# Optimization experiments

Measured on AMD Instinct MI355X. Metric: run time of the kernel, lower is better.

The kernel has to match this reference:

```python
import jax, jax.numpy as jnp
import numpy as np

WINDOW = 4
EPS = 1e-5


def setup_inputs() -> dict:
    key = jax.random.key(0)
    ks = jax.random.split(key, 12)
    B, T, D = 2, 4096, 1024
    H = D // 2
    s = 0.02
    return {
        "x": jax.random.normal(ks[0], (B, T, D), dtype=jnp.float32),
        # tension_net: Linear(2D -> D/2), SiLU, Linear(D/2 -> 1). Weights stored [in, out].
        "w1": jax.random.normal(ks[1], (2 * D, H), dtype=jnp.float32) * s,
        "b1": jnp.zeros((H,), dtype=jnp.float32),
        "w2": jax.random.normal(ks[2], (H, 1), dtype=jnp.float32) * s,
        "b2": jnp.zeros((1,), dtype=jnp.float32),
        # wv: Linear(D -> D)
        "wv_w": jax.random.normal(ks[3], (D, D), dtype=jnp.float32) * s,
        "wv_b": jnp.zeros((D,), dtype=jnp.float32),
        # merge: Linear(2D -> D)
        "merge_w": jax.random.normal(ks[4], (2 * D, D), dtype=jnp.float32) * s,
        "merge_b": jnp.zeros((D,), dtype=jnp.float32),
        # LayerNorm(D)
        "gamma": jnp.ones((D,), dtype=jnp.float32),
        "beta": jnp.zeros((D,), dtype=jnp.float32),
    }


def reference(x, w1, b1, w2, b2, wv_w, wv_b, merge_w, merge_b, gamma, beta):
    B, T, D = x.shape
    W = WINDOW
    # Causal sliding-window neighbor gather: nb[:, t, w] = x[:, t-w-1] if t-w-1 >= 0 else 0.
    idx = jnp.arange(T)[:, None] - jnp.arange(W)[None, :] - 1          # [T, W]
    valid = (idx >= 0)                                                  # [T, W]
    nb = jnp.take(x, jnp.clip(idx, 0, None), axis=1)                   # [B, T, W, D]
    nb = jnp.where(valid[None, :, :, None], nb, jnp.zeros((), x.dtype))
    # Pairwise tension gate: tiny MLP on [h_t, nb].
    h_t = jnp.broadcast_to(x[:, :, None, :], (B, T, W, D))
    pair = jnp.concatenate([h_t, nb], axis=-1)                          # [B, T, W, 2D]
    hid = jax.nn.silu(jnp.einsum('btwe,eh->btwh', pair, w1) + b1)       # [B, T, W, D/2]
    tau = jax.nn.sigmoid((jnp.einsum('btwh,ho->btwo', hid, w2) + b2)[..., 0])  # [B, T, W]
    # Value projection of neighbors (note: zero-padded neighbors still get wv bias, matching torch).
    v = jnp.einsum('btwd,de->btwe', nb, wv_w) + wv_b                    # [B, T, W, D]
    msg = jnp.einsum('btw,btwd->btd', tau, v)                           # [B, T, D]
    # Merge + LayerNorm.
    y = jnp.einsum('bte,ed->btd', jnp.concatenate([x, msg], axis=-1), merge_w) + merge_b
    mu = jnp.mean(y, axis=-1, keepdims=True)
    var = jnp.mean(jnp.square(y - mu), axis=-1, keepdims=True)
    y = (y - mu) * jax.lax.rsqrt(var + EPS) * gamma + beta
    return y
```

## Files before the change

kernel.cpp:

```cpp
#include <hip/hip_runtime.h>
#include <hip/hip_bf16.h>

#define TT 4096
#define TD 1024
#define TM 8192
#define CN 3072
#define EPS 1e-5f

typedef __bf16 bf16;
typedef __bf16 bf16x4 __attribute__((ext_vector_type(4)));
typedef __bf16 bf16x8 __attribute__((ext_vector_type(8)));
typedef float  f32x4  __attribute__((ext_vector_type(4)));

#define GLOBAL_AS __attribute__((address_space(1)))
#define LDS_AS    __attribute__((address_space(3)))

__global__ __launch_bounds__(256) void prep_kernel(const float* __restrict__ x,
                                                   const float* __restrict__ w1,
                                                   const float* __restrict__ wv_w,
                                                   const float* __restrict__ wv_b,
                                                   const float* __restrict__ merge_w,
                                                   bf16* __restrict__ Xbf,
                                                   bf16* __restrict__ BigBT,
                                                   bf16* __restrict__ Amb,
                                                   bf16* __restrict__ WvBf,
                                                   float* __restrict__ cvecP) {
    __shared__ float tile[32][33];
    int b = blockIdx.x;
    const int tid = threadIdx.x;

    if (b < 16) {
        const int j = (b & 3) * 256 + tid;
        const int e0 = (b >> 2) * 256;
        const float* col = merge_w + (size_t)(1024 + e0) * 1024 + j;
        float acc = 0.f;
#pragma unroll 32
        for (int e = 0; e < 256; ++e) acc += wv_b[e0 + e] * col[(size_t)e * 1024];
        cvecP[(b >> 2) * 1024 + j] = acc;
        return;
    }
    b -= 16;
    if (b < 8192) {
        int i = b * 256 + tid;
        float4 v = ((const float4*)x)[i];
        bf16x4 o; o[0] = (bf16)v.x; o[1] = (bf16)v.y; o[2] = (bf16)v.z; o[3] = (bf16)v.w;
        *(bf16x4*)(Xbf + (size_t)i * 4) = o;
        return;
    }
    b -= 8192;

    const float* src; bf16* dst; int srcN, tilesX, dstOff;
    if (b < 512)       {            src = w1;                        srcN = 512;  tilesX = 16; dst = BigBT; dstOff = 0;    }
    else if (b < 1024) { b -= 512;  src = w1 + (size_t)1024 * 512;   srcN = 512;  tilesX = 16; dst = BigBT; dstOff = 512;  }
    else if (b < 2048) { b -= 1024; src = merge_w;                   srcN = 1024; tilesX = 32; dst = BigBT; dstOff = 2048; }
    else if (b < 3072) { b -= 2048; src = merge_w + (size_t)1024 * 1024; srcN = 1024; tilesX = 32; dst = Amb; dstOff = 0; }
    else {
        b -= 3072;
        int i = b * 256 + tid;
        float4 v = ((const float4*)wv_w)[i];
        bf16x4 o; o[0] = (bf16)v.x; o[1] = (bf16)v.y; o[2] = (bf16)v.z; o[3] = (bf16)v.w;
        *(bf16x4*)(WvBf + (size_t)i * 4) = o;
        return;
    }
    int n0 = (b % tilesX) * 32, k0 = (b / tilesX) * 32;
    int tx = tid & 31, ty = tid >> 5;
#pragma unroll
    for (int r = 0; r < 32; r += 8)
        tile[ty + r][tx] = src[(size_t)(k0 + ty + r) * srcN + n0 + tx];
    __syncthreads();
#pragma unroll
    for (int r = 0; r < 32; r += 8)
        dst[(size_t)(dstOff + n0 + ty + r) * 1024 + k0 + tx] = (bf16)tile[tx][ty + r];
}

__global__ __launch_bounds__(256) void wprime_kernel(const bf16* __restrict__ Amb,
                                                     const bf16* __restrict__ WvBf,
                                                     bf16* __restrict__ Wout,
                                                     const float* __restrict__ cvecP,
                                                     float* __restrict__ cvec) {
    int b = blockIdx.x;
    if (b == 256) {
        int j = threadIdx.x * 4;
        float4 s0 = *(const float4*)(cvecP + j);
        float4 s1 = *(const float4*)(cvecP + 1024 + j);
        float4 s2 = *(const float4*)(cvecP + 2048 + j);
        float4 s3 = *(const float4*)(cvecP + 3072 + j);
        float4 o = {s0.x + s1.x + s2.x + s3.x, s0.y + s1.y + s2.y + s3.y,
                    s0.z + s1.z + s2.z + s3.z, s0.w + s1.w + s2.w + s3.w};
        *(float4*)(cvec + j) = o;
        return;
    }
    __shared__ bf16 As[64 * 64];
    __shared__ bf16 Bs[64 * 64];
    const int m0 = (b >> 4) * 64;
    const int n0 = (b & 15) * 64;
    const int tid = threadIdx.x;
    const int wave = tid >> 6, lane = tid & 63;
    const int wr = (wave >> 1) * 32, wc = (wave & 1) * 32;
    const int lrow = lane & 15, cbase = lane >> 4;
    const int sw = lrow & 7;

    f32x4 acc[2][2] = {};

    for (int k0 = 0; k0 < 1024; k0 += 64) {
        __syncthreads();
#pragma unroll
        for (int c = 0; c < 2; ++c) {
            int e = (c * 256 + tid) * 8;
            int row = e >> 6;
            int q = (e >> 3) & 7;
            int gcol = ((q ^ (row & 7)) << 3);
            const bf16* ga = Amb  + (size_t)(m0 + row) * 1024 + k0 + gcol;
            const bf16* gb = WvBf + (size_t)(n0 + row) * 1024 + k0 + gcol;
            __builtin_amdgcn_global_load_lds((const GLOBAL_AS void*)ga,
                                             (LDS_AS void*)(As + e), 16, 0, 0);
            __builtin_amdgcn_global_load_lds((const GLOBAL_AS void*)gb,
                                             (LDS_AS void*)(Bs + e), 16, 0, 0);
        }
        __syncthreads();

#pragma unroll
        for (int kk = 0; kk < 2; ++kk) {
            const int qo = ((cbase + kk * 4) ^ sw) << 3;
            bf16x8 af[2], bfr[2];
#pragma unroll
            for (int i = 0; i < 2; ++i) {
                af[i]  = *(const bf16x8*)(As + (wr + i * 16 + lrow) * 64 + qo);
                bfr[i] = *(const bf16x8*)(Bs + (wc + i * 16 + lrow) * 64 + qo);
            }
#pragma unroll
            for (int i = 0; i < 2; ++i)
#pragma unroll
                for (int j = 0; j < 2; ++j)
                    acc[i][j] = __builtin_amdgcn_mfma_f32_16x16x32_bf16(af[i], bfr[j], acc[i][j], 0, 0, 0);
        }
    }

    const int lr = (lane >> 4) * 4, lc = lane & 15;
#pragma unroll
    for (int i = 0; i < 2; ++i)
#pragma unroll
        for (int j = 0; j < 2; ++j)
#pragma unroll
            for (int r = 0; r < 4; ++r)
                Wout[(size_t)(m0 + wr + i * 16 + lr + r) * 1024 + (n0 + wc + j * 16 + lc)]
                    = (bf16)acc[i][j][r];
}

#define MFMA16(a, b, c) __builtin_amdgcn_mfma_f32_16x16x32_bf16((a), (b), (c), 0, 0, 0)

#define STAGE_A(BUF, T, L0, L1) do {                                              \
    _Pragma("unroll")                                                             \
    for (int ld_ = (L0); ld_ < (L1); ++ld_) {                                     \
        const bf16* ga_ = aBase + (size_t)(ld_ * 32) * 1024 + (T) * 64;           \
        __builtin_amdgcn_global_load_lds((const GLOBAL_AS void*)ga_,              \
            (LDS_AS void*)(SMEM + (BUF) * 28672 + ld_ * 2048 + tid * 8), 16, 0, 0); \
    } } while (0)

#define STAGE_B(BUF, T, L0, L1) do {                                              \
    _Pragma("unroll")                                                             \
    for (int ld_ = (L0); ld_ < (L1); ++ld_) {                                     \
        const bf16* gb_ = bBase + (size_t)(ld_ * 32) * 1024 + (T) * 64;           \
        __builtin_amdgcn_global_load_lds((const GLOBAL_AS void*)gb_,              \
            (LDS_AS void*)(SMEM + (BUF) * 28672 + 16384 + ld_ * 2048 + tid * 8), 16, 0, 0); \
    } } while (0)

#define AF(BUF, I, KK) (*(const bf16x8*)(SMEM + (BUF) * 28672 +                   \
    (wm * 128 + (I) * 16 + lrow) * 64 + (((cbase + (KK) * 4) ^ sw) << 3)))
#define BF(BUF, J, KK) (*(const bf16x8*)(SMEM + (BUF) * 28672 + 16384 +           \
    (wn * 96 + (J) * 16 + lrow) * 64 + (((cbase + (KK) * 4) ^ sw) << 3)))

#define NOSTAGE do {} while (0)
#define NOGATE  do {} while (0)
#define GATE0 do { asm volatile("s_waitcnt vmcnt(0)" ::: "memory");               \
                   __builtin_amdgcn_sched_barrier(0); } while (0)

#define PH(BUF, KK, H, RDB, STAGE, GATE) do {                                     \
    if (RDB) {                                                                    \
        _Pragma("unroll")                                                         \
        for (int j = 0; j < 6; ++j) bfr[j] = BF(BUF, j, KK);                      \
    }                                                                             \
    bf16x8 a0_ = AF(BUF, (H) * 4 + 0, KK);                                        \
    bf16x8 a1_ = AF(BUF, (H) * 4 + 1, KK);                                        \
    bf16x8 a2_ = AF(BUF, (H) * 4 + 2, KK);                                        \
    bf16x8 a3_ = AF(BUF, (H) * 4 + 3, KK);                                        \
    STAGE;                                                                        \
    __builtin_amdgcn_s_barrier();                                                 \
    __builtin_amdgcn_sched_barrier(0);                                            \
    __builtin_amdgcn_s_setprio(1);                                                \
    _Pragma("unroll")                                                             \
    for (int j = 0; j < 6; ++j) {                                                 \
        acc[(H) * 4 + 0][j] = MFMA16(a0_, bfr[j], acc[(H) * 4 + 0][j]);           \
        acc[(H) * 4 + 1][j] = MFMA16(a1_, bfr[j], acc[(H) * 4 + 1][j]);           \
        acc[(H) * 4 + 2][j] = MFMA16(a2_, bfr[j], acc[(H) * 4 + 2][j]);           \
        acc[(H) * 4 + 3][j] = MFMA16(a3_, bfr[j], acc[(H) * 4 + 3][j]);           \
    }                                                                             \
    __builtin_amdgcn_s_setprio(0);                                                \
    GATE;                                                                         \
    __builtin_amdgcn_s_barrier();                                                 \
    __builtin_amdgcn_sched_barrier(0);                                            \
} while (0)

#define TILE(BUF, S0, S1, S2, G3)                                                 \
    PH(BUF, 0, 0, 1, S0, NOGATE);                                                 \
    PH(BUF, 0, 1, 0, S1, NOGATE);                                                 \
    PH(BUF, 1, 0, 1, S2, NOGATE);                                                 \
    PH(BUF, 1, 1, 0, NOSTAGE, G3);

__global__ __launch_bounds__(256, 1) void gemm_big(const bf16* __restrict__ A,
                                                   const bf16* __restrict__ BT,
                                                   bf16* __restrict__ C) {
    __shared__ __align__(16) bf16 SMEM[57344];
    const int NB = 3072, K = 1024;

    const int L = blockIdx.x;
    const int m0 = (L >> 4) * 256;
    const int n0 = ((L & 7) * 2 + ((L >> 3) & 1)) * 192;
    const int tid = threadIdx.x;
    const int wave = tid >> 6, lane = tid & 63;
    const int wm = wave >> 1;
    const int wn = wave & 1;
    const int lrow = lane & 15, cbase = lane >> 4;
    const int sw = lrow & 7;

    const int r0 = tid >> 3;
    const int c0 = ((tid & 7) ^ ((tid >> 3) & 7)) << 3;
    const bf16* aBase = A  + (size_t)(m0 + r0) * K + c0;
    const bf16* bBase = BT + (size_t)(n0 + r0) * K + c0;

    f32x4 acc[8][6] = {};
    bf16x8 bfr[6];

    STAGE_A(0, 0, 0, 8);
    STAGE_B(0, 0, 0, 6);
    asm volatile("s_waitcnt vmcnt(0)" ::: "memory");
    __builtin_amdgcn_sched_barrier(0);
    __builtin_amdgcn_s_barrier();
    __builtin_amdgcn_sched_barrier(0);

    for (int i = 0; i < 7; ++i) {
        const int t1 = 2 * i + 1, t2 = 2 * i + 2;
        TILE(0, STAGE_A(1, t1, 0, 4), STAGE_A(1, t1, 4, 8), STAGE_B(1, t1, 0, 6), GATE0);
        TILE(1, STAGE_A(0, t2, 0, 4), STAGE_A(0, t2, 4, 8), STAGE_B(0, t2, 0, 6), GATE0);
    }
    TILE(0, STAGE_A(1, 15, 0, 4), STAGE_A(1, 15, 4, 8), STAGE_B(1, 15, 0, 6), GATE0);
    TILE(1, NOSTAGE, NOSTAGE, NOSTAGE, NOGATE);

    __syncthreads();
    bf16* ep = SMEM + wave * 6656;
    const int lr = (lane >> 4) * 4, lc = lane & 15;
#pragma unroll
    for (int h = 0; h < 2; ++h) {
#pragma unroll
        for (int ii = 0; ii < 4; ++ii)
#pragma unroll
            for (int j = 0; j < 6; ++j)
#pragma unroll
                for (int r = 0; r < 4; ++r)
                    ep[(ii * 16 + lr + r) * 104 + (j * 16 + lc)]
                        = (bf16)acc[h * 4 + ii][j][r];
        __syncthreads();
        bf16* Cw = C + (size_t)(m0 + wm * 128 + h * 64) * NB + n0 + wn * 96;
#pragma unroll
        for (int p = 0; p < 8; ++p) {
            int R = p * 8 + (lane >> 3);
            int Ccol = (lane & 7) * 8;
            bf16x8 v = *(const bf16x8*)(ep + R * 104 + Ccol);
            *(bf16x8*)(Cw + (size_t)R * NB + Ccol) = v;
        }
#pragma unroll
        for (int p = 0; p < 4; ++p) {
            int R = p * 16 + (lane >> 2);
            int Ccol = 64 + (lane & 3) * 8;
            bf16x8 v = *(const bf16x8*)(ep + R * 104 + Ccol);
            *(bf16x8*)(Cw + (size_t)R * NB + Ccol) = v;
        }
        __syncthreads();
    }
}

__global__ __launch_bounds__(256) void final_kernel(const bf16* __restrict__ C,
                                                    const float* __restrict__ b1,
                                                    const float* __restrict__ b2,
                                                    const float* __restrict__ w2,
                                                    const float* __restrict__ cvec,
                                                    const float* __restrict__ merge_b,
                                                    const float* __restrict__ gamma,
                                                    const float* __restrict__ beta,
                                                    float* __restrict__ out) {
    const int wave = threadIdx.x >> 6, lane = threadIdx.x & 63;
    const int row = blockIdx.x * 4 + wave;
    const int t = row & (TT - 1);
    const bf16* Crow = C + (size_t)row * CN;

    const int h0 = lane * 8;
    bf16x8 u8 = *(const bf16x8*)(Crow + h0);
    float4 b1a = *(const float4*)(b1 + h0), b1b = *(const float4*)(b1 + h0 + 4);
    float4 w2a = *(const float4*)(w2 + h0), w2b = *(const float4*)(w2 + h0 + 4);
    float u[8] = {(float)u8[0] + b1a.x, (float)u8[1] + b1a.y,
                  (float)u8[2] + b1a.z, (float)u8[3] + b1a.w,
                  (float)u8[4] + b1b.x, (float)u8[5] + b1b.y,
                  (float)u8[6] + b1b.z, (float)u8[7] + b1b.w};
    const float w2v[8] = {w2a.x, w2a.y, w2a.z, w2a.w, w2b.x, w2b.y, w2b.z, w2b.w};

    float partial[4];
#pragma unroll
    for (int w = 0; w < 4; ++w) {
        float p = 0.f;
        if (t >= w + 1) {
            bf16x8 v8 = *(const bf16x8*)(C + (size_t)(row - w - 1) * CN + 512 + h0);
#pragma unroll
            for (int k = 0; k < 8; ++k) {
                float z = u[k] + (float)v8[k];
                p += (z / (1.f + __expf(-z))) * w2v[k];
            }
        } else {
#pragma unroll
            for (int k = 0; k < 8; ++k) {
                float z = u[k];
                p += (z / (1.f + __expf(-z))) * w2v[k];
            }
        }
        partial[w] = p;
    }
#pragma unroll
    for (int w = 0; w < 4; ++w)
#pragma unroll
        for (int off = 1; off < 64; off <<= 1)
            partial[w] += __shfl_xor(partial[w], off, 64);

    const float bias2 = b2[0];
    float taus[4];
#pragma unroll
    for (int w = 0; w < 4; ++w)
        taus[w] = 1.f / (1.f + __expf(-(partial[w] + bias2)));
    const float tsum = taus[0] + taus[1] + taus[2] + taus[3];

    const int d0 = lane * 16;
    bf16x8 y1a = *(const bf16x8*)(Crow + 2048 + d0);
    bf16x8 y1b = *(const bf16x8*)(Crow + 2048 + d0 + 8);
    float v[16];
#pragma unroll
    for (int k = 0; k < 8; ++k) { v[k] = (float)y1a[k]; v[8 + k] = (float)y1b[k]; }
#pragma unroll
    for (int q = 0; q < 4; ++q) {
        float4 cv = *(const float4*)(cvec + d0 + q * 4);
        float4 mb = *(const float4*)(merge_b + d0 + q * 4);
        v[q*4+0] += tsum * cv.x + mb.x; v[q*4+1] += tsum * cv.y + mb.y;
        v[q*4+2] += tsum * cv.z + mb.z; v[q*4+3] += tsum * cv.w + mb.w;
    }
#pragma unroll
    for (int w = 0; w < 4; ++w) {
        if (t >= w + 1) {
            const bf16* Pn = C + (size_t)(row - w - 1) * CN + 1024 + d0;
            bf16x8 pa = *(const bf16x8*)Pn;
            bf16x8 pb = *(const bf16x8*)(Pn + 8);
#pragma unroll
            for (int k = 0; k < 8; ++k) {
                v[k] += taus[w] * (float)pa[k];
                v[8 + k] += taus[w] * (float)pb[k];
            }
        }
    }

    float s = 0.f, ss = 0.f;
#pragma unroll
    for (int k = 0; k < 16; ++k) { s += v[k]; ss += v[k] * v[k]; }
#pragma unroll
    for (int off = 1; off < 64; off <<= 1) {
        s  += __shfl_xor(s, off, 64);
        ss += __shfl_xor(ss, off, 64);
    }
    const float mu = s * (1.f / TD);
    const float var = ss * (1.f / TD) - mu * mu;
    const float r = rsqrtf(var + EPS);

#pragma unroll
    for (int q = 0; q < 4; ++q) {
        float4 g  = *(const float4*)(gamma + d0 + q * 4);
        float4 bt = *(const float4*)(beta + d0 + q * 4);
        float4 o;
        o.x = (v[q*4+0] - mu) * r * g.x + bt.x;
        o.y = (v[q*4+1] - mu) * r * g.y + bt.y;
        o.z = (v[q*4+2] - mu) * r * g.z + bt.z;
        o.w = (v[q*4+3] - mu) * r * g.w + bt.w;
        *(float4*)(out + (size_t)row * TD + d0 + q * 4) = o;
    }
}

extern "C" void kernel_launch(void* const* d_in, const int* in_sizes, int n_in,
                              void* d_out, int out_size, void* d_ws, size_t ws_size,
                              hipStream_t stream) {
    const float* x       = (const float*)d_in[0];
    const float* w1      = (const float*)d_in[1];
    const float* b1      = (const float*)d_in[2];
    const float* w2      = (const float*)d_in[3];
    const float* b2      = (const float*)d_in[4];
    const float* wv_w    = (const float*)d_in[5];
    const float* wv_b    = (const float*)d_in[6];
    const float* merge_w = (const float*)d_in[7];
    const float* merge_b = (const float*)d_in[8];
    const float* gamma   = (const float*)d_in[9];
    const float* beta    = (const float*)d_in[10];
    float* out = (float*)d_out;

    char* ws = (char*)d_ws;
    bf16*  Xbf   = (bf16*)ws;  ws += (size_t)TM * 1024 * 2;
    bf16*  BigBT = (bf16*)ws;  ws += (size_t)CN * 1024 * 2;
    bf16*  Amb   = (bf16*)ws;  ws += (size_t)1024 * 1024 * 2;
    bf16*  WvBf  = (bf16*)ws;  ws += (size_t)1024 * 1024 * 2;
    float* cvecP = (float*)ws; ws += (size_t)4 * 1024 * 4;
    float* cvec  = (float*)ws; ws += (size_t)1024 * 4;
    bf16*  Cbuf  = (bf16*)ws;

    prep_kernel<<<12304, 256, 0, stream>>>(x, w1, wv_w, wv_b, merge_w,
                                           Xbf, BigBT, Amb, WvBf, cvecP);

    wprime_kernel<<<257, 256, 0, stream>>>(Amb, WvBf, BigBT + (size_t)1024 * 1024,
                                           cvecP, cvec);

    gemm_big<<<512, 256, 0, stream>>>(Xbf, BigBT, Cbuf);

    final_kernel<<<TM / 4, 256, 0, stream>>>(Cbuf, b1, b2, w2, cvec, merge_b,
                                             gamma, beta, out);
}
```

Measured before the change: 202.9 us.

## Use 512-thread blocks with 8 waves splitting the GEMM tile

```diff
diff --git a/kernel.cpp b/kernel.cpp
--- a/kernel.cpp
+++ b/kernel.cpp
@@ -149,24 +149,24 @@
 
 #define MFMA16(a, b, c) __builtin_amdgcn_mfma_f32_16x16x32_bf16((a), (b), (c), 0, 0, 0)
 
-#define STAGE_A(BUF, T, L0, L1) do {                                              \
+#define STAGE_A(BUF, T) do {                                                      \
     _Pragma("unroll")                                                             \
-    for (int ld_ = (L0); ld_ < (L1); ++ld_) {                                     \
-        const bf16* ga_ = aBase + (size_t)(ld_ * 32) * 1024 + (T) * 64;           \
+    for (int ld_ = 0; ld_ < 4; ++ld_) {                                           \
+        const bf16* ga_ = aBase + (size_t)(ld_ * 64) * 1024 + (T) * 64;           \
         __builtin_amdgcn_global_load_lds((const GLOBAL_AS void*)ga_,              \
-            (LDS_AS void*)(SMEM + (BUF) * 28672 + ld_ * 2048 + tid * 8), 16, 0, 0); \
+            (LDS_AS void*)(SMEM + (BUF) * 28672 + ld_ * 4096 + tid * 8), 16, 0, 0); \
     } } while (0)
 
-#define STAGE_B(BUF, T, L0, L1) do {                                              \
+#define STAGE_B(BUF, T) do {                                                      \
     _Pragma("unroll")                                                             \
-    for (int ld_ = (L0); ld_ < (L1); ++ld_) {                                     \
-        const bf16* gb_ = bBase + (size_t)(ld_ * 32) * 1024 + (T) * 64;           \
+    for (int ld_ = 0; ld_ < 3; ++ld_) {                                           \
+        const bf16* gb_ = bBase + (size_t)(ld_ * 64) * 1024 + (T) * 64;           \
         __builtin_amdgcn_global_load_lds((const GLOBAL_AS void*)gb_,              \
-            (LDS_AS void*)(SMEM + (BUF) * 28672 + 16384 + ld_ * 2048 + tid * 8), 16, 0, 0); \
+            (LDS_AS void*)(SMEM + (BUF) * 28672 + 16384 + ld_ * 4096 + tid * 8), 16, 0, 0); \
     } } while (0)
 
 #define AF(BUF, I, KK) (*(const bf16x8*)(SMEM + (BUF) * 28672 +                   \
-    (wm * 128 + (I) * 16 + lrow) * 64 + (((cbase + (KK) * 4) ^ sw) << 3)))
+    (wm * 64 + (I) * 16 + lrow) * 64 + (((cbase + (KK) * 4) ^ sw) << 3)))
 #define BF(BUF, J, KK) (*(const bf16x8*)(SMEM + (BUF) * 28672 + 16384 +           \
     (wn * 96 + (J) * 16 + lrow) * 64 + (((cbase + (KK) * 4) ^ sw) << 3)))
 
@@ -180,20 +180,16 @@
         _Pragma("unroll")                                                         \
         for (int j = 0; j < 6; ++j) bfr[j] = BF(BUF, j, KK);                      \
     }                                                                             \
-    bf16x8 a0_ = AF(BUF, (H) * 4 + 0, KK);                                        \
-    bf16x8 a1_ = AF(BUF, (H) * 4 + 1, KK);                                        \
-    bf16x8 a2_ = AF(BUF, (H) * 4 + 2, KK);                                        \
-    bf16x8 a3_ = AF(BUF, (H) * 4 + 3, KK);                                        \
+    bf16x8 a0_ = AF(BUF, (H) * 2 + 0, KK);                                        \
+    bf16x8 a1_ = AF(BUF, (H) * 2 + 1, KK);                                        \
     STAGE;                                                                        \
     __builtin_amdgcn_s_barrier();                                                 \
     __builtin_amdgcn_sched_barrier(0);                                            \
     __builtin_amdgcn_s_setprio(1);                                                \
     _Pragma("unroll")                                                             \
     for (int j = 0; j < 6; ++j) {                                                 \
-        acc[(H) * 4 + 0][j] = MFMA16(a0_, bfr[j], acc[(H) * 4 + 0][j]);           \
-        acc[(H) * 4 + 1][j] = MFMA16(a1_, bfr[j], acc[(H) * 4 + 1][j]);           \
-        acc[(H) * 4 + 2][j] = MFMA16(a2_, bfr[j], acc[(H) * 4 + 2][j]);           \
-        acc[(H) * 4 + 3][j] = MFMA16(a3_, bfr[j], acc[(H) * 4 + 3][j]);           \
+        acc[(H) * 2 + 0][j] = MFMA16(a0_, bfr[j], acc[(H) * 2 + 0][j]);           \
+        acc[(H) * 2 + 1][j] = MFMA16(a1_, bfr[j], acc[(H) * 2 + 1][j]);           \
     }                                                                             \
     __builtin_amdgcn_s_setprio(0);                                                \
     GATE;                                                                         \
@@ -201,13 +197,13 @@
     __builtin_amdgcn_sched_barrier(0);                                            \
 } while (0)
 
-#define TILE(BUF, S0, S1, S2, G3)                                                 \
-    PH(BUF, 0, 0, 1, S0, NOGATE);                                                 \
-    PH(BUF, 0, 1, 0, S1, NOGATE);                                                 \
-    PH(BUF, 1, 0, 1, S2, NOGATE);                                                 \
+#define TILE(BUF, SA, SB, G3)                                                     \
+    PH(BUF, 0, 0, 1, SA, NOGATE);                                                 \
+    PH(BUF, 0, 1, 0, SB, NOGATE);                                                 \
+    PH(BUF, 1, 0, 1, NOSTAGE, NOGATE);                                            \
     PH(BUF, 1, 1, 0, NOSTAGE, G3);
 
-__global__ __launch_bounds__(256, 1) void gemm_big(const bf16* __restrict__ A,
+__global__ __launch_bounds__(512, 2) void gemm_big(const bf16* __restrict__ A,
                                                    const bf16* __restrict__ BT,
                                                    bf16* __restrict__ C) {
     __shared__ __align__(16) bf16 SMEM[57344];
@@ -228,11 +224,11 @@
     const bf16* aBase = A  + (size_t)(m0 + r0) * K + c0;
     const bf16* bBase = BT + (size_t)(n0 + r0) * K + c0;
 
-    f32x4 acc[8][6] = {};
+    f32x4 acc[4][6] = {};
     bf16x8 bfr[6];
 
-    STAGE_A(0, 0, 0, 8);
-    STAGE_B(0, 0, 0, 6);
+    STAGE_A(0, 0);
+    STAGE_B(0, 0);
     asm volatile("s_waitcnt vmcnt(0)" ::: "memory");
     __builtin_amdgcn_sched_barrier(0);
     __builtin_amdgcn_s_barrier();
@@ -240,42 +236,38 @@
 
     for (int i = 0; i < 7; ++i) {
         const int t1 = 2 * i + 1, t2 = 2 * i + 2;
-        TILE(0, STAGE_A(1, t1, 0, 4), STAGE_A(1, t1, 4, 8), STAGE_B(1, t1, 0, 6), GATE0);
-        TILE(1, STAGE_A(0, t2, 0, 4), STAGE_A(0, t2, 4, 8), STAGE_B(0, t2, 0, 6), GATE0);
-    }
-    TILE(0, STAGE_A(1, 15, 0, 4), STAGE_A(1, 15, 4, 8), STAGE_B(1, 15, 0, 6), GATE0);
-    TILE(1, NOSTAGE, NOSTAGE, NOSTAGE, NOGATE);
+        TILE(0, STAGE_A(1, t1), STAGE_B(1, t1), GATE0);
+        TILE(1, STAGE_A(0, t2), STAGE_B(0, t2), GATE0);
+    }
+    TILE(0, STAGE_A(1, 15), STAGE_B(1, 15), GATE0);
+    TILE(1, NOSTAGE, NOSTAGE, NOGATE);
 
     __syncthreads();
     bf16* ep = SMEM + wave * 6656;
     const int lr = (lane >> 4) * 4, lc = lane & 15;
 #pragma unroll
-    for (int h = 0; h < 2; ++h) {
-#pragma unroll
-        for (int ii = 0; ii < 4; ++ii)
-#pragma unroll
-            for (int j = 0; j < 6; ++j)
-#pragma unroll
-                for (int r = 0; r < 4; ++r)
-                    ep[(ii * 16 + lr + r) * 104 + (j * 16 + lc)]
-                        = (bf16)acc[h * 4 + ii][j][r];
-        __syncthreads();
-        bf16* Cw = C + (size_t)(m0 + wm * 128 + h * 64) * NB + n0 + wn * 96;
-#pragma unroll
-        for (int p = 0; p < 8; ++p) {
-            int R = p * 8 + (lane >> 3);
-            int Ccol = (lane & 7) * 8;
-            bf16x8 v = *(const bf16x8*)(ep + R * 104 + Ccol);
-            *(bf16x8*)(Cw + (size_t)R * NB + Ccol) = v;
-        }
-#pragma unroll
-        for (int p = 0; p < 4; ++p) {
-            int R = p * 16 + (lane >> 2);
-            int Ccol = 64 + (lane & 3) * 8;
-            bf16x8 v = *(const bf16x8*)(ep + R * 104 + Ccol);
-            *(bf16x8*)(Cw + (size_t)R * NB + Ccol) = v;
-        }
-        __syncthreads();
+    for (int i = 0; i < 4; ++i)
+#pragma unroll
+        for (int j = 0; j < 6; ++j)
+#pragma unroll
+            for (int r = 0; r < 4; ++r)
+                ep[(i * 16 + lr + r) * 104 + (j * 16 + lc)] = (bf16)acc[i][j][r];
+    __syncthreads();
+
+    bf16* Cw = C + (size_t)(m0 + wm * 64) * NB + n0 + wn * 96;
+#pragma unroll
+    for (int p = 0; p < 8; ++p) {
+        int R = p * 8 + (lane >> 3);
+        int Ccol = (lane & 7) * 8;
+        bf16x8 v = *(const bf16x8*)(ep + R * 104 + Ccol);
+        *(bf16x8*)(Cw + (size_t)R * NB + Ccol) = v;
+    }
+#pragma unroll
+    for (int p = 0; p < 4; ++p) {
+        int R = p * 16 + (lane >> 2);
+        int Ccol = 64 + (lane & 3) * 8;
+        bf16x8 v = *(const bf16x8*)(ep + R * 104 + Ccol);
+        *(bf16x8*)(Cw + (size_t)R * NB + Ccol) = v;
     }
 }
 
@@ -419,7 +411,7 @@
     wprime_kernel<<<257, 256, 0, stream>>>(Amb, WvBf, BigBT + (size_t)1024 * 1024,
                                            cvecP, cvec);
 
-    gemm_big<<<512, 256, 0, stream>>>(Xbf, BigBT, Cbuf);
+    gemm_big<<<512, 512, 0, stream>>>(Xbf, BigBT, Cbuf);
 
     final_kernel<<<TM / 4, 256, 0, stream>>>(Cbuf, b1, b2, w2, cvec, merge_b,
                                              gamma, beta, out);
```

Result: faster. 198.8 us (-2.0%).
